# Kernel tuning notes

Hardware: AMD Instinct MI355X
Metric: run time of the kernel (lower is better)

Reference implementation:

```python
import jax, jax.numpy as jnp
import numpy as np

N = 50000   # nodes
E = 800000  # edges (avg degree 16)
H = 8       # heads
D = 64      # per-head feature dim


def setup_inputs() -> dict:
    key = jax.random.key(0)
    k1, k2, k3, k4 = jax.random.split(key, 4)
    q = jax.random.normal(k1, (N, H, D), dtype=jnp.float32)
    k = jax.random.normal(k2, (N, H, D), dtype=jnp.float32)
    v = jax.random.normal(k3, (N, H, D), dtype=jnp.float32)
    edge_index = jax.random.randint(k4, (2, E), 0, N, dtype=jnp.int32)
    return {"q": q, "k": k, "v": v, "edge_index": edge_index, "latent": 0}


def reference(q, k, v, edge_index, latent):
    A = edge_index[0]  # destination node per edge [E]
    B = edge_index[1]  # source node per edge [E]
    # per-edge scores: q[A] [E,H,D] @ k[B]^T [E,D,H] -> [E,H,H]
    score_e = jnp.einsum('ehd,egd->ehg', q[A], k[B])
    # mean-aggregate edges into destination nodes (vectorized over both head axes;
    # equivalent to the per-head MeanAggregation loop in the original)
    seg_sum = jax.ops.segment_sum(score_e, A, num_segments=N)          # [N,H,H]
    cnt = jax.ops.segment_sum(jnp.ones((A.shape[0],), score_e.dtype), A, num_segments=N)
    score = seg_sum / jnp.maximum(cnt, 1.0)[:, None, None]             # empty segments -> 0
    score = jax.nn.softmax(score, axis=-1)                              # [N,H,H]
    out = jnp.einsum('nhg,ngd->nhd', score, v)                          # [N,H,D]
    return (out, score) if latent else out
```

## Files before the change

kernel.cpp:

```cpp
#include <hip/hip_runtime.h>
#include <hip/hip_fp16.h>


#define ROW 512
#define LPAD 68
#define EPB 2048

typedef float f4 __attribute__((ext_vector_type(4)));
typedef unsigned int u4 __attribute__((ext_vector_type(4)));


__device__ __forceinline__ void dev_convert(const float* __restrict__ k,
                                            unsigned int* __restrict__ kh, int i) {
    const f4* src = (const f4*)k + (size_t)i * 2;
    f4 x0 = __builtin_nontemporal_load(src);
    f4 x1 = __builtin_nontemporal_load(src + 1);
    union { __half2 h2; unsigned int u; } c0, c1, c2, c3;
    c0.h2 = __floats2half2_rn(x0.x, x0.y);
    c1.h2 = __floats2half2_rn(x0.z, x0.w);
    c2.h2 = __floats2half2_rn(x1.x, x1.y);
    c3.h2 = __floats2half2_rn(x1.z, x1.w);
    u4 o = {c0.u, c1.u, c2.u, c3.u};
    ((u4*)kh)[i] = o;
}

__device__ __forceinline__ int excl_scan_256(int x, int t, int* scr) {
    int lane = t & 63, w = t >> 6;
    int v = x;
    #pragma unroll
    for (int off = 1; off < 64; off <<= 1) {
        int u = __shfl_up(v, off, 64);
        if (lane >= off) v += u;
    }
    __syncthreads();
    if (lane == 63) scr[w] = v;
    __syncthreads();
    int base = 0;
    #pragma unroll
    for (int i = 0; i < 4; ++i) if (i < w) base += scr[i];
    return base + v - x;
}

__device__ __forceinline__ void acc8(u4 x, f4& a0, f4& a1) {
    union { unsigned int u; __half2 h; } p0{x.x}, p1{x.y}, p2{x.z}, p3{x.w};
    a0.x += __low2float(p0.h); a0.y += __high2float(p0.h);
    a0.z += __low2float(p1.h); a0.w += __high2float(p1.h);
    a1.x += __low2float(p2.h); a1.y += __high2float(p2.h);
    a1.z += __low2float(p3.h); a1.w += __high2float(p3.h);
}


__global__ __launch_bounds__(256) void w_convhist(
    const int* __restrict__ A, int* __restrict__ bh, int E, int HB, int NB,
    const float* __restrict__ k, unsigned int* __restrict__ kh, int total8)
{
    __shared__ int h[256];
    int blk = blockIdx.x, t = threadIdx.x;
    if (blk >= HB) {
        int i = (blk - HB) * 256 + t;
        if (i < total8) dev_convert(k, kh, i);
        return;
    }
    h[t] = 0;
    __syncthreads();
    int base = blk * EPB + t * 8;
    if (base + 8 <= E) {
        int4 a0 = *(const int4*)(A + base);
        int4 a1 = *(const int4*)(A + base + 4);
        atomicAdd(&h[a0.x >> 8], 1); atomicAdd(&h[a0.y >> 8], 1);
        atomicAdd(&h[a0.z >> 8], 1); atomicAdd(&h[a0.w >> 8], 1);
        atomicAdd(&h[a1.x >> 8], 1); atomicAdd(&h[a1.y >> 8], 1);
        atomicAdd(&h[a1.z >> 8], 1); atomicAdd(&h[a1.w >> 8], 1);
    } else {
        for (int j = 0; j < 8; ++j) { int i = base + j; if (i < E) atomicAdd(&h[A[i] >> 8], 1); }
    }
    __syncthreads();
    if (t < NB) bh[t * HB + blk] = h[t];
}

__global__ __launch_bounds__(256) void w_rowsum(const int* __restrict__ bh,
                                                int* __restrict__ rowsum, int HB) {
    __shared__ int scr[4];
    int g = blockIdx.x, t = threadIdx.x;
    int s = 0;
    for (int c = t; c < HB; c += 256) s += bh[g * HB + c];
    #pragma unroll
    for (int off = 32; off; off >>= 1) s += __shfl_down(s, off, 64);
    int lane = t & 63, w = t >> 6;
    if (lane == 0) scr[w] = s;
    __syncthreads();
    if (t == 0) rowsum[g] = scr[0] + scr[1] + scr[2] + scr[3];
}

__global__ __launch_bounds__(256) void w_scanbase(const int* __restrict__ rowsum,
                                                  int* __restrict__ rowbase,
                                                  int* __restrict__ offsets,
                                                  int NB, int N, int E) {
    __shared__ int scr[4];
    int t = threadIdx.x;
    int x = (t < NB) ? rowsum[t] : 0;
    int p = excl_scan_256(x, t, scr);
    if (t <= NB) rowbase[t] = p;
    if (t == 0) offsets[N] = E;
}

__global__ __launch_bounds__(256) void w_rowscan(int* __restrict__ bh,
                                                 const int* __restrict__ rowbase, int HB) {
    __shared__ int scr[4];
    int g = blockIdx.x, t = threadIdx.x;
    int j0 = 2 * t, j1 = 2 * t + 1;
    int c0 = (j0 < HB) ? bh[g * HB + j0] : 0;
    int c1 = (j1 < HB) ? bh[g * HB + j1] : 0;
    int p = excl_scan_256(c0 + c1, t, scr);
    int base = rowbase[g];
    if (j0 < HB) bh[g * HB + j0] = base + p;
    if (j1 < HB) bh[g * HB + j1] = base + p + c0;
}

__global__ __launch_bounds__(256) void w_scatter(
    const int* __restrict__ A, const int* __restrict__ Bs, const int* __restrict__ bh,
    int* __restrict__ tmp, int E, int HB, int NB)
{
    __shared__ int cur[256];
    int blk = blockIdx.x, t = threadIdx.x;
    if (t < NB) cur[t] = bh[t * HB + blk];
    __syncthreads();
    int base = blk * EPB + t * 8;
    bool bal = ((((unsigned long long)(size_t)Bs) & 15) == 0);
    if (base + 8 <= E && bal) {
        int4 a0 = *(const int4*)(A + base);
        int4 a1 = *(const int4*)(A + base + 4);
        int4 b0 = *(const int4*)(Bs + base);
        int4 b1 = *(const int4*)(Bs + base + 4);
        int as[8] = {a0.x, a0.y, a0.z, a0.w, a1.x, a1.y, a1.z, a1.w};
        int bs[8] = {b0.x, b0.y, b0.z, b0.w, b1.x, b1.y, b1.z, b1.w};
        #pragma unroll
        for (int j = 0; j < 8; ++j) {
            int pos = atomicAdd(&cur[as[j] >> 8], 1);
            tmp[pos] = ((as[j] & 255) << 24) | bs[j];
        }
    } else {
        for (int j = 0; j < 8; ++j) {
            int i = base + j;
            if (i < E) {
                int a = A[i], b = Bs[i];
                int pos = atomicAdd(&cur[a >> 8], 1);
                tmp[pos] = ((a & 255) << 24) | b;
            }
        }
    }
}

__global__ __launch_bounds__(256) void w_build(
    const int* __restrict__ rowbase, const int* __restrict__ tmp,
    int* __restrict__ offsets, int* __restrict__ srcs, int N, int E, int NB)
{
    __shared__ int cnt[256];
    __shared__ int scr[4];
    int g = blockIdx.x, t = threadIdx.x;
    int s = rowbase[g];
    int e = rowbase[g + 1];
    cnt[t] = 0;
    __syncthreads();
    for (int i = s + t; i < e; i += 256) atomicAdd(&cnt[(tmp[i] >> 24) & 255], 1);
    __syncthreads();
    int val = cnt[t];
    int p = excl_scan_256(val, t, scr);
    int n0 = (g << 8) + t;
    if (n0 < N) offsets[n0] = s + p;
    __syncthreads();
    cnt[t] = s + p;
    __syncthreads();
    for (int i = s + t; i < e; i += 256) {
        int wv = tmp[i];
        int pos = atomicAdd(&cnt[(wv >> 24) & 255], 1);
        srcs[pos] = wv & 0xFFFFFF;
    }
}

__global__ __launch_bounds__(256) void w_node16(
    const float* __restrict__ q, const unsigned int* __restrict__ kh,
    const float* __restrict__ v, const int* __restrict__ offsets,
    const int* __restrict__ srcs, float* __restrict__ out, int N)
{
    __shared__ float lds[4][2 * 8 * LPAD + 64 + 8];
    int lane = threadIdx.x & 63;
    int wid  = threadIdx.x >> 6;
    int n = blockIdx.x * 4 + wid;
    bool active = n < N;

    float* qs = &lds[wid][0];
    float* ks = qs + 8 * LPAD;
    float* ps = ks + 8 * LPAD;

    int start = 0, end = 0;
    if (active) {
        start = __builtin_amdgcn_readfirstlane(offsets[n]);
        end   = __builtin_amdgcn_readfirstlane(offsets[n + 1]);
        int r0 = lane >> 4;
        int dq = (lane & 15) * 4;
        const f4* qn = (const f4*)(q + (size_t)n * ROW);
        f4 q0 = __builtin_nontemporal_load(qn + lane);
        f4 q1 = __builtin_nontemporal_load(qn + 64 + lane);
        *(f4*)(qs + r0 * LPAD + dq)       = q0;
        *(f4*)(qs + (r0 + 4) * LPAD + dq) = q1;
    }

    const u4* kh4 = (const u4*)kh;
    f4 a0 = {0.f, 0.f, 0.f, 0.f}, a1 = {0.f, 0.f, 0.f, 0.f};
    int e = start;

    int b0, b1, b2, b3, b4, b5, b6, b7;
    if (e + 8 <= end) {
        b0 = srcs[e];     b1 = srcs[e + 1]; b2 = srcs[e + 2]; b3 = srcs[e + 3];
        b4 = srcs[e + 4]; b5 = srcs[e + 5]; b6 = srcs[e + 6]; b7 = srcs[e + 7];
    }
    while (e + 8 <= end) {
        u4 x0 = kh4[(size_t)b0 * 64 + lane];
        u4 x1 = kh4[(size_t)b1 * 64 + lane];
        u4 x2 = kh4[(size_t)b2 * 64 + lane];
        u4 x3 = kh4[(size_t)b3 * 64 + lane];
        u4 x4 = kh4[(size_t)b4 * 64 + lane];
        u4 x5 = kh4[(size_t)b5 * 64 + lane];
        u4 x6 = kh4[(size_t)b6 * 64 + lane];
        u4 x7 = kh4[(size_t)b7 * 64 + lane];
        e += 8;
        if (e + 8 <= end) {
            b0 = srcs[e];     b1 = srcs[e + 1]; b2 = srcs[e + 2]; b3 = srcs[e + 3];
            b4 = srcs[e + 4]; b5 = srcs[e + 5]; b6 = srcs[e + 6]; b7 = srcs[e + 7];
        }
        acc8(x0, a0, a1); acc8(x1, a0, a1); acc8(x2, a0, a1); acc8(x3, a0, a1);
        acc8(x4, a0, a1); acc8(x5, a0, a1); acc8(x6, a0, a1); acc8(x7, a0, a1);
    }
    if (e + 4 <= end) {
        int c0 = srcs[e], c1 = srcs[e + 1], c2 = srcs[e + 2], c3 = srcs[e + 3];
        u4 x0 = kh4[(size_t)c0 * 64 + lane];
        u4 x1 = kh4[(size_t)c1 * 64 + lane];
        u4 x2 = kh4[(size_t)c2 * 64 + lane];
        u4 x3 = kh4[(size_t)c3 * 64 + lane];
        acc8(x0, a0, a1); acc8(x1, a0, a1); acc8(x2, a0, a1); acc8(x3, a0, a1);
        e += 4;
    }
    for (; e < end; ++e) {
        u4 x = kh4[(size_t)srcs[e] * 64 + lane];
        acc8(x, a0, a1);
    }

    if (active) {
        int g = lane >> 3;
        int dbase = (lane & 7) * 8;
        *(f4*)(ks + g * LPAD + dbase)     = a0;
        *(f4*)(ks + g * LPAD + dbase + 4) = a1;
    }
    __syncthreads();

    if (active) {
        int h = lane >> 3, g = lane & 7;
        const f4* qrow = (const f4*)(qs + h * LPAD);
        const f4* krow = (const f4*)(ks + g * LPAD);
        float acc = 0.f;
        #pragma unroll
        for (int i = 0; i < 16; ++i) {
            f4 qa = qrow[i];
            f4 kb = krow[i];
            acc += qa.x * kb.x + qa.y * kb.y + qa.z * kb.z + qa.w * kb.w;
        }
        int cnt = end - start;
        float score = acc / (float)((cnt > 0) ? cnt : 1);
        float mx = score;
        #pragma unroll
        for (int off = 1; off < 8; off <<= 1)
            mx = fmaxf(mx, __shfl_xor(mx, off, 8));
        float ex = __expf(score - mx);
        float sm = ex;
        #pragma unroll
        for (int off = 1; off < 8; off <<= 1)
            sm += __shfl_xor(sm, off, 8);
        ps[h * 8 + g] = ex / sm;
    }
    __syncthreads();

    if (active) {
        int h0 = lane >> 4;
        int dbase = (lane & 15) * 4;
        const float* vb = v + (size_t)n * ROW;
        f4 o0 = {0.f, 0.f, 0.f, 0.f}, o1 = {0.f, 0.f, 0.f, 0.f};
        #pragma unroll
        for (int g = 0; g < 8; ++g) {
            f4 vg = __builtin_nontemporal_load((const f4*)(vb + g * 64 + dbase));
            float p0 = ps[h0 * 8 + g];
            float p1 = ps[(h0 + 4) * 8 + g];
            o0 += p0 * vg;
            o1 += p1 * vg;
        }
        f4* ob = (f4*)(out + (size_t)n * ROW);
        __builtin_nontemporal_store(o0, ob + lane);
        __builtin_nontemporal_store(o1, ob + 64 + lane);
    }
}

__global__ __launch_bounds__(256) void w_node32(
    const float* __restrict__ q, const float* __restrict__ k,
    const float* __restrict__ v, const int* __restrict__ offsets,
    const int* __restrict__ srcs, float* __restrict__ out, int N)
{
    __shared__ float lds[4][2 * 8 * LPAD + 64 + 8];
    int lane = threadIdx.x & 63;
    int wid  = threadIdx.x >> 6;
    int n = blockIdx.x * 4 + wid;
    bool active = n < N;

    float* qs = &lds[wid][0];
    float* ks = qs + 8 * LPAD;
    float* ps = ks + 8 * LPAD;

    int start = 0, end = 0;
    if (active) { start = offsets[n]; end = offsets[n + 1]; }

    f4 a0 = {0.f, 0.f, 0.f, 0.f}, a1 = {0.f, 0.f, 0.f, 0.f};
    for (int e = start; e < end; ++e) {
        int b = srcs[e];
        const f4* kb = (const f4*)(k + (size_t)b * ROW);
        f4 x0 = kb[lane];
        f4 x1 = kb[64 + lane];
        a0 += x0; a1 += x1;
    }

    if (active) {
        int r0 = lane >> 4;
        int dbase = (lane & 15) * 4;
        *(f4*)(ks + r0 * LPAD + dbase)       = a0;
        *(f4*)(ks + (r0 + 4) * LPAD + dbase) = a1;
        const f4* qn = (const f4*)(q + (size_t)n * ROW);
        f4 q0 = qn[lane], q1 = qn[64 + lane];
        *(f4*)(qs + r0 * LPAD + dbase)       = q0;
        *(f4*)(qs + (r0 + 4) * LPAD + dbase) = q1;
    }
    __syncthreads();

    if (active) {
        int h = lane >> 3, g = lane & 7;
        const f4* qrow = (const f4*)(qs + h * LPAD);
        const f4* krow = (const f4*)(ks + g * LPAD);
        float acc = 0.f;
        #pragma unroll
        for (int i = 0; i < 16; ++i) {
            f4 qa = qrow[i];
            f4 kb = krow[i];
            acc += qa.x * kb.x + qa.y * kb.y + qa.z * kb.z + qa.w * kb.w;
        }
        int cnt = end - start;
        float score = acc / (float)((cnt > 0) ? cnt : 1);
        float mx = score;
        #pragma unroll
        for (int off = 1; off < 8; off <<= 1)
            mx = fmaxf(mx, __shfl_xor(mx, off, 8));
        float ex = __expf(score - mx);
        float sm = ex;
        #pragma unroll
        for (int off = 1; off < 8; off <<= 1)
            sm += __shfl_xor(sm, off, 8);
        ps[h * 8 + g] = ex / sm;
    }
    __syncthreads();

    if (active) {
        int h0 = lane >> 4;
        int dbase = (lane & 15) * 4;
        const float* vb = v + (size_t)n * ROW;
        f4 o0 = {0.f, 0.f, 0.f, 0.f}, o1 = {0.f, 0.f, 0.f, 0.f};
        #pragma unroll
        for (int g = 0; g < 8; ++g) {
            f4 vg = *(const f4*)(vb + g * 64 + dbase);
            float p0 = ps[h0 * 8 + g];
            float p1 = ps[(h0 + 4) * 8 + g];
            o0 += p0 * vg;
            o1 += p1 * vg;
        }
        f4* ob = (f4*)(out + (size_t)n * ROW);
        ob[lane]      = o0;
        ob[64 + lane] = o1;
    }
}

extern "C" void kernel_launch(void* const* d_in, const int* in_sizes, int n_in,
                              void* d_out, int out_size, void* d_ws, size_t ws_size,
                              hipStream_t stream) {
    const float* q  = (const float*)d_in[0];
    const float* k  = (const float*)d_in[1];
    const float* v  = (const float*)d_in[2];
    const int*   ei = (const int*)d_in[3];

    int N = in_sizes[0] / ROW;
    int E = in_sizes[3] / 2;
    const int* A  = ei;
    const int* Bs = ei + E;

    int HB = (E + EPB - 1) / EPB;
    int NB = (N + 255) >> 8;

    int* offsets = (int*)d_ws;
    int* srcs    = offsets + (N + 1);
    int* tmp     = srcs + E;
    int* bh      = tmp + E;
    int* rowsum  = bh + (size_t)NB * HB;
    int* rowbase = rowsum + NB;
    size_t int_words = (size_t)(N + 1) + 2 * (size_t)E + (size_t)NB * HB + NB + (NB + 1);
    size_t kh_off = ((int_words * 4 + 255) & ~(size_t)255);
    unsigned int* kh = (unsigned int*)((char*)d_ws + kh_off);
    bool use_f16 = ws_size >= kh_off + (size_t)N * ROW * 2;
    int total8 = N * (ROW / 8);
    int CONVB  = (total8 + 255) / 256;
    float* out = (float*)d_out;

    w_convhist<<<HB + (use_f16 ? CONVB : 0), 256, 0, stream>>>(A, bh, E, HB, NB, k, kh, total8);
    w_rowsum<<<NB, 256, 0, stream>>>(bh, rowsum, HB);
    w_scanbase<<<1, 256, 0, stream>>>(rowsum, rowbase, offsets, NB, N, E);
    w_rowscan<<<NB, 256, 0, stream>>>(bh, rowbase, HB);
    w_scatter<<<HB, 256, 0, stream>>>(A, Bs, bh, tmp, E, HB, NB);
    w_build<<<NB, 256, 0, stream>>>(rowbase, tmp, offsets, srcs, N, E, NB);
    if (use_f16)
        w_node16<<<(N + 3) / 4, 256, 0, stream>>>(q, kh, v, offsets, srcs, out, N);
    else
        w_node32<<<(N + 3) / 4, 256, 0, stream>>>(q, k, v, offsets, srcs, out, N);
}
```

Measured before the change: 425.8 us.

## Quantize gathered keys to int8 with per-head scales instead of fp16

After: 381.4 us. 1.12x faster.

```diff
diff --git a/kernel.cpp b/kernel.cpp
--- a/kernel.cpp
+++ b/kernel.cpp
@@ -10,18 +10,42 @@
 typedef unsigned int u4 __attribute__((ext_vector_type(4)));
 
 
-__device__ __forceinline__ void dev_convert(const float* __restrict__ k,
-                                            unsigned int* __restrict__ kh, int i) {
-    const f4* src = (const f4*)k + (size_t)i * 2;
-    f4 x0 = __builtin_nontemporal_load(src);
-    f4 x1 = __builtin_nontemporal_load(src + 1);
-    union { __half2 h2; unsigned int u; } c0, c1, c2, c3;
-    c0.h2 = __floats2half2_rn(x0.x, x0.y);
-    c1.h2 = __floats2half2_rn(x0.z, x0.w);
-    c2.h2 = __floats2half2_rn(x1.x, x1.y);
-    c3.h2 = __floats2half2_rn(x1.z, x1.w);
-    u4 o = {c0.u, c1.u, c2.u, c3.u};
-    ((u4*)kh)[i] = o;
+__device__ __forceinline__ void dev_quant(const float* __restrict__ k,
+                                          unsigned int* __restrict__ kb8,
+                                          float* __restrict__ scl,
+                                          int n, int lane) {
+    const f4* src = (const f4*)(k + (size_t)n * ROW);
+    f4 x0 = __builtin_nontemporal_load(src + lane * 2);
+    f4 x1 = __builtin_nontemporal_load(src + lane * 2 + 1);
+    float m = fmaxf(fmaxf(fmaxf(fabsf(x0.x), fabsf(x0.y)), fmaxf(fabsf(x0.z), fabsf(x0.w))),
+                    fmaxf(fmaxf(fabsf(x1.x), fabsf(x1.y)), fmaxf(fabsf(x1.z), fabsf(x1.w))));
+    #pragma unroll
+    for (int off = 1; off < 8; off <<= 1)
+        m = fmaxf(m, __shfl_xor(m, off, 8));
+    float inv = (m > 0.f) ? 127.0f / m : 0.f;
+    int r0 = (int)rintf(x0.x * inv), r1 = (int)rintf(x0.y * inv);
+    int r2 = (int)rintf(x0.z * inv), r3 = (int)rintf(x0.w * inv);
+    int r4 = (int)rintf(x1.x * inv), r5 = (int)rintf(x1.y * inv);
+    int r6 = (int)rintf(x1.z * inv), r7 = (int)rintf(x1.w * inv);
+    unsigned lo = (unsigned)(r0 & 255) | ((unsigned)(r1 & 255) << 8) |
+                  ((unsigned)(r2 & 255) << 16) | ((unsigned)(r3 & 255) << 24);
+    unsigned hi = (unsigned)(r4 & 255) | ((unsigned)(r5 & 255) << 8) |
+                  ((unsigned)(r6 & 255) << 16) | ((unsigned)(r7 & 255) << 24);
+    uint2 w; w.x = lo; w.y = hi;
+    ((uint2*)kb8)[(size_t)n * 64 + lane] = w;
+    if ((lane & 7) == 0) scl[n * 8 + (lane >> 3)] = m * (1.0f / 127.0f);
+}
+
+__device__ __forceinline__ void acci8(uint2 w, float s, f4& a0, f4& a1) {
+    int lo = (int)w.x, hi = (int)w.y;
+    a0.x += s * (float)(char)(lo);
+    a0.y += s * (float)(char)(lo >> 8);
+    a0.z += s * (float)(char)(lo >> 16);
+    a0.w += s * (float)(lo >> 24);
+    a1.x += s * (float)(char)(hi);
+    a1.y += s * (float)(char)(hi >> 8);
+    a1.z += s * (float)(char)(hi >> 16);
+    a1.w += s * (float)(hi >> 24);
 }
 
 __device__ __forceinline__ int excl_scan_256(int x, int t, int* scr) {
@@ -41,24 +65,17 @@
     return base + v - x;
 }
 
-__device__ __forceinline__ void acc8(u4 x, f4& a0, f4& a1) {
-    union { unsigned int u; __half2 h; } p0{x.x}, p1{x.y}, p2{x.z}, p3{x.w};
-    a0.x += __low2float(p0.h); a0.y += __high2float(p0.h);
-    a0.z += __low2float(p1.h); a0.w += __high2float(p1.h);
-    a1.x += __low2float(p2.h); a1.y += __high2float(p2.h);
-    a1.z += __low2float(p3.h); a1.w += __high2float(p3.h);
-}
-
-
-__global__ __launch_bounds__(256) void w_convhist(
+
+__global__ __launch_bounds__(256) void w_quanthist(
     const int* __restrict__ A, int* __restrict__ bh, int E, int HB, int NB,
-    const float* __restrict__ k, unsigned int* __restrict__ kh, int total8)
+    const float* __restrict__ k, unsigned int* __restrict__ kb8,
+    float* __restrict__ scl, int N)
 {
     __shared__ int h[256];
     int blk = blockIdx.x, t = threadIdx.x;
     if (blk >= HB) {
-        int i = (blk - HB) * 256 + t;
-        if (i < total8) dev_convert(k, kh, i);
+        int nb = (blk - HB) * 4 + (t >> 6);
+        if (nb < N) dev_quant(k, kb8, scl, nb, t & 63);
         return;
     }
     h[t] = 0;
@@ -178,16 +195,18 @@
     }
 }
 
-__global__ __launch_bounds__(256) void w_node16(
-    const float* __restrict__ q, const unsigned int* __restrict__ kh,
-    const float* __restrict__ v, const int* __restrict__ offsets,
-    const int* __restrict__ srcs, float* __restrict__ out, int N)
+__global__ __launch_bounds__(256) void w_node8(
+    const float* __restrict__ q, const unsigned int* __restrict__ kb8,
+    const float* __restrict__ scl, const float* __restrict__ v,
+    const int* __restrict__ offsets, const int* __restrict__ srcs,
+    float* __restrict__ out, int N)
 {
     __shared__ float lds[4][2 * 8 * LPAD + 64 + 8];
     int lane = threadIdx.x & 63;
     int wid  = threadIdx.x >> 6;
     int n = blockIdx.x * 4 + wid;
     bool active = n < N;
+    int g8 = lane >> 3;
 
     float* qs = &lds[wid][0];
     float* ks = qs + 8 * LPAD;
@@ -206,7 +225,7 @@
         *(f4*)(qs + (r0 + 4) * LPAD + dq) = q1;
     }
 
-    const u4* kh4 = (const u4*)kh;
+    const uint2* kr = (const uint2*)kb8;
     f4 a0 = {0.f, 0.f, 0.f, 0.f}, a1 = {0.f, 0.f, 0.f, 0.f};
     int e = start;
 
@@ -216,34 +235,45 @@
         b4 = srcs[e + 4]; b5 = srcs[e + 5]; b6 = srcs[e + 6]; b7 = srcs[e + 7];
     }
     while (e + 8 <= end) {
-        u4 x0 = kh4[(size_t)b0 * 64 + lane];
-        u4 x1 = kh4[(size_t)b1 * 64 + lane];
-        u4 x2 = kh4[(size_t)b2 * 64 + lane];
-        u4 x3 = kh4[(size_t)b3 * 64 + lane];
-        u4 x4 = kh4[(size_t)b4 * 64 + lane];
-        u4 x5 = kh4[(size_t)b5 * 64 + lane];
-        u4 x6 = kh4[(size_t)b6 * 64 + lane];
-        u4 x7 = kh4[(size_t)b7 * 64 + lane];
+        uint2 x0 = kr[(size_t)b0 * 64 + lane];
+        uint2 x1 = kr[(size_t)b1 * 64 + lane];
+        uint2 x2 = kr[(size_t)b2 * 64 + lane];
+        uint2 x3 = kr[(size_t)b3 * 64 + lane];
+        uint2 x4 = kr[(size_t)b4 * 64 + lane];
+        uint2 x5 = kr[(size_t)b5 * 64 + lane];
+        uint2 x6 = kr[(size_t)b6 * 64 + lane];
+        uint2 x7 = kr[(size_t)b7 * 64 + lane];
+        float s0 = scl[b0 * 8 + g8], s1 = scl[b1 * 8 + g8];
+        float s2 = scl[b2 * 8 + g8], s3 = scl[b3 * 8 + g8];
+        float s4 = scl[b4 * 8 + g8], s5 = scl[b5 * 8 + g8];
+        float s6 = scl[b6 * 8 + g8], s7 = scl[b7 * 8 + g8];
         e += 8;
         if (e + 8 <= end) {
             b0 = srcs[e];     b1 = srcs[e + 1]; b2 = srcs[e + 2]; b3 = srcs[e + 3];
             b4 = srcs[e + 4]; b5 = srcs[e + 5]; b6 = srcs[e + 6]; b7 = srcs[e + 7];
         }
-        acc8(x0, a0, a1); acc8(x1, a0, a1); acc8(x2, a0, a1); acc8(x3, a0, a1);
-        acc8(x4, a0, a1); acc8(x5, a0, a1); acc8(x6, a0, a1); acc8(x7, a0, a1);
+        acci8(x0, s0, a0, a1); acci8(x1, s1, a0, a1);
+        acci8(x2, s2, a0, a1); acci8(x3, s3, a0, a1);
+        acci8(x4, s4, a0, a1); acci8(x5, s5, a0, a1);
+        acci8(x6, s6, a0, a1); acci8(x7, s7, a0, a1);
     }
     if (e + 4 <= end) {
         int c0 = srcs[e], c1 = srcs[e + 1], c2 = srcs[e + 2], c3 = srcs[e + 3];
-        u4 x0 = kh4[(size_t)c0 * 64 + lane];
-        u4 x1 = kh4[(size_t)c1 * 64 + lane];
-        u4 x2 = kh4[(size_t)c2 * 64 + lane];
-        u4 x3 = kh4[(size_t)c3 * 64 + lane];
-        acc8(x0, a0, a1); acc8(x1, a0, a1); acc8(x2, a0, a1); acc8(x3, a0, a1);
+        uint2 x0 = kr[(size_t)c0 * 64 + lane];
+        uint2 x1 = kr[(size_t)c1 * 64 + lane];
+        uint2 x2 = kr[(size_t)c2 * 64 + lane];
+        uint2 x3 = kr[(size_t)c3 * 64 + lane];
+        float s0 = scl[c0 * 8 + g8], s1 = scl[c1 * 8 + g8];
+        float s2 = scl[c2 * 8 + g8], s3 = scl[c3 * 8 + g8];
+        acci8(x0, s0, a0, a1); acci8(x1, s1, a0, a1);
+        acci8(x2, s2, a0, a1); acci8(x3, s3, a0, a1);
         e += 4;
     }
     for (; e < end; ++e) {
-        u4 x = kh4[(size_t)srcs[e] * 64 + lane];
-        acc8(x, a0, a1);
+        int b = srcs[e];
+        uint2 x = kr[(size_t)b * 64 + lane];
+        float s = scl[b * 8 + g8];
+        acci8(x, s, a0, a1);
     }
 
     if (active) {
@@ -405,22 +435,24 @@
     int* bh      = tmp + E;
     int* rowsum  = bh + (size_t)NB * HB;
     int* rowbase = rowsum + NB;
-    size_t int_words = (size_t)(N + 1) + 2 * (size_t)E + (size_t)NB * HB + NB + (NB + 1);
-    size_t kh_off = ((int_words * 4 + 255) & ~(size_t)255);
-    unsigned int* kh = (unsigned int*)((char*)d_ws + kh_off);
-    bool use_f16 = ws_size >= kh_off + (size_t)N * ROW * 2;
-    int total8 = N * (ROW / 8);
-    int CONVB  = (total8 + 255) / 256;
+    float* scl   = (float*)(rowbase + NB + 1);
+    size_t int_words = (size_t)(N + 1) + 2 * (size_t)E + (size_t)NB * HB + NB + (NB + 1)
+                     + (size_t)N * 8;
+    size_t kb8_off = ((int_words * 4 + 255) & ~(size_t)255);
+    unsigned int* kb8 = (unsigned int*)((char*)d_ws + kb8_off);
+    bool use_i8 = ws_size >= kb8_off + (size_t)N * 512;
+    int QUANTB = (N + 3) / 4;
     float* out = (float*)d_out;
 
-    w_convhist<<<HB + (use_f16 ? CONVB : 0), 256, 0, stream>>>(A, bh, E, HB, NB, k, kh, total8);
+    w_quanthist<<<HB + (use_i8 ? QUANTB : 0), 256, 0, stream>>>(
+        A, bh, E, HB, NB, k, kb8, scl, use_i8 ? N : 0);
     w_rowsum<<<NB, 256, 0, stream>>>(bh, rowsum, HB);
     w_scanbase<<<1, 256, 0, stream>>>(rowsum, rowbase, offsets, NB, N, E);
     w_rowscan<<<NB, 256, 0, stream>>>(bh, rowbase, HB);
     w_scatter<<<HB, 256, 0, stream>>>(A, Bs, bh, tmp, E, HB, NB);
     w_build<<<NB, 256, 0, stream>>>(rowbase, tmp, offsets, srcs, N, E, NB);
-    if (use_f16)
-        w_node16<<<(N + 3) / 4, 256, 0, stream>>>(q, kh, v, offsets, srcs, out, N);
+    if (use_i8)
+        w_node8<<<(N + 3) / 4, 256, 0, stream>>>(q, kb8, scl, v, offsets, srcs, out, N);
     else
         w_node32<<<(N + 3) / 4, 256, 0, stream>>>(q, k, v, offsets, srcs, out, N);
 }
```
